# Kernel tuning notes

Hardware: AMD Instinct MI355X
Metric: run time of the kernel (lower is better)

Reference implementation:

```python
import jax, jax.numpy as jnp
import numpy as np

WS = 8          # window size
NUM_HEADS = 3
DIM = 96
HIDDEN = int(DIM * 2.0)
LN_EPS = 1e-5


def _rel_pos_index(ws):
    coords = np.stack(np.meshgrid(np.arange(ws), np.arange(ws), indexing='ij'))  # (2,ws,ws)
    cf = coords.reshape(2, -1)                          # (2, N)
    rel = cf[:, :, None] - cf[:, None, :]               # (2, N, N)
    rel = rel.transpose(1, 2, 0).astype(np.int64)       # (N, N, 2)
    rel[:, :, 0] += ws - 1
    rel[:, :, 1] += ws - 1
    rel[:, :, 0] *= 2 * ws - 1
    return jnp.asarray(rel.sum(-1))                     # (N, N)


def _layernorm(x, g, b):
    mu = jnp.mean(x, axis=-1, keepdims=True)
    var = jnp.mean(jnp.square(x - mu), axis=-1, keepdims=True)
    return (x - mu) * jax.lax.rsqrt(var + LN_EPS) * g + b


def setup_inputs() -> dict:
    key = jax.random.key(0)
    ks = jax.random.split(key, 10)
    C = DIM
    std = 0.02
    return {
        'x': jax.random.normal(ks[0], (8, C, 256, 256), dtype=jnp.float32),
        'qkv_w': jax.random.normal(ks[1], (3 * C, C), dtype=jnp.float32) * std,
        'qkv_b': jnp.zeros((3 * C,), dtype=jnp.float32),
        'proj_w': jax.random.normal(ks[2], (C, C), dtype=jnp.float32) * std,
        'proj_b': jnp.zeros((C,), dtype=jnp.float32),
        'rpb_table': jax.random.normal(ks[3], ((2 * WS - 1) ** 2, NUM_HEADS), dtype=jnp.float32) * std,
        'norm1_g': jnp.ones((C,), dtype=jnp.float32),
        'norm1_b': jnp.zeros((C,), dtype=jnp.float32),
        'norm2_g': jnp.ones((C,), dtype=jnp.float32),
        'norm2_b': jnp.zeros((C,), dtype=jnp.float32),
        'fc1_w': jax.random.normal(ks[4], (HIDDEN, C), dtype=jnp.float32) * std,
        'fc1_b': jnp.zeros((HIDDEN,), dtype=jnp.float32),
        'fc2_w': jax.random.normal(ks[5], (C, HIDDEN), dtype=jnp.float32) * std,
        'fc2_b': jnp.zeros((C,), dtype=jnp.float32),
        'H': 256,
        'W': 256,
    }


def reference(x, qkv_w, qkv_b, proj_w, proj_b, rpb_table,
              norm1_g, norm1_b, norm2_g, norm2_b,
              fc1_w, fc1_b, fc2_w, fc2_b, H, W):
    B, C, Hc, Wc = x.shape
    ws = WS
    nh, nw = H // ws, W // ws
    N = ws * ws
    heads = NUM_HEADS
    hd = C // heads

    # window partition: (B,C,H,W) -> (B*nh*nw, N, C)
    xp = jnp.transpose(x, (0, 2, 3, 1))
    xw = xp.reshape(B, nh, ws, nw, ws, C).transpose(0, 1, 3, 2, 4, 5)
    xw = xw.reshape(B * nh * nw, N, C)

    xw = _layernorm(xw, norm1_g, norm1_b)

    # window attention
    B_ = B * nh * nw
    qkv = xw @ qkv_w.T + qkv_b                                  # (B_, N, 3C)
    qkv = qkv.reshape(B_, N, 3, heads, hd).transpose(2, 0, 3, 1, 4)
    q, k, v = qkv[0], qkv[1], qkv[2]                            # (B_, h, N, d)
    q = q * (hd ** -0.5)
    attn = jnp.einsum('bhnd,bhmd->bhnm', q, k)                  # (B_, h, N, N)
    rpi = _rel_pos_index(ws)                                    # (N, N)
    bias = rpb_table[rpi.reshape(-1)].reshape(N, N, heads).transpose(2, 0, 1)
    attn = jax.nn.softmax(attn + bias[None], axis=-1)
    out = jnp.einsum('bhnm,bhmd->bhnd', attn, v)                # (B_, h, N, d)
    out = out.transpose(0, 2, 1, 3).reshape(B_, N, C)
    out = out @ proj_w.T + proj_b

    # norm2 + MLP (note: original applies them sequentially, single residual at end)
    out = _layernorm(out, norm2_g, norm2_b)
    h = jax.nn.gelu(out @ fc1_w.T + fc1_b, approximate=False)
    out = h @ fc2_w.T + fc2_b

    # window merge + residual
    out = out.reshape(B, nh, nw, ws, ws, C).transpose(0, 5, 1, 3, 2, 4)
    out = out.reshape(B, C, H, W)
    return out + x
```

## Files before the change

kernel.cpp:

```cpp
#include <hip/hip_runtime.h>
#include <hip/hip_bf16.h>

using bf16 = __hip_bfloat16;
typedef short short8  __attribute__((ext_vector_type(8)));
typedef short short4v __attribute__((ext_vector_type(4)));
typedef float f32x4   __attribute__((ext_vector_type(4)));

static __device__ __forceinline__ float b2f(bf16 v){ return __bfloat162float(v); }
static __device__ __forceinline__ bf16  f2b(float v){ return __float2bfloat16(v); }
static __device__ __forceinline__ float s2f(short s){ return __bfloat162float(__builtin_bit_cast(bf16, s)); }
static __device__ __forceinline__ short f2s(float f){ return __builtin_bit_cast(short, __float2bfloat16(f)); }

static __device__ __forceinline__ short8 ldw8(const float* __restrict__ p){
  const float4 u = *(const float4*)(p);
  const float4 v = *(const float4*)(p + 4);
  short8 r;
  r[0]=f2s(u.x); r[1]=f2s(u.y); r[2]=f2s(u.z); r[3]=f2s(u.w);
  r[4]=f2s(v.x); r[5]=f2s(v.y); r[6]=f2s(v.z); r[7]=f2s(v.w);
  return r;
}

#define MFMA16(a,b,c) __builtin_amdgcn_mfma_f32_16x16x32_bf16((a),(b),(c),0,0,0)

constexpr int TPB = 256;
constexpr float EPS = 1e-5f;
constexpr float QSC = 0.17677669529663687f;

constexpr int WQ_OFF  = 0;
constexpr int WPJ_OFF = 27648;
constexpr int WF1_OFF = 36864;
constexpr int WF2_OFF = 55296;
constexpr int WTOT    = 73728;
constexpr int BTAB_BYTE_OFF = 147456;
constexpr size_t WS_NEEDED = 147456 + 49152;

constexpr int R0_OFF = 0;
constexpr int R1_OFF = 26624;
constexpr int R2_OFF = 53248;
constexpr int SMEM_BYTES = 80896;

__global__ void init_ws_kernel(
    const float* __restrict__ qkvw, const float* __restrict__ projw,
    const float* __restrict__ fc1w, const float* __restrict__ fc2w,
    const float* __restrict__ rpb,
    bf16* __restrict__ wbf, float* __restrict__ btab)
{
  const int i = blockIdx.x * 256 + threadIdx.x;
  if (i < WTOT){
    float v;
    if (i < WPJ_OFF)      v = qkvw[i];
    else if (i < WF1_OFF) v = projw[i - WPJ_OFF];
    else if (i < WF2_OFF) v = fc1w[i - WF1_OFF];
    else                  v = fc2w[i - WF2_OFF];
    wbf[i] = f2b(v);
  }
  if (i < 3*64*64){
    const int h   = i >> 12;
    const int row = (i >> 6) & 63;
    const int col = i & 63;
    const int rel = ((row>>3) - (col>>3) + 7)*15 + ((row&7) - (col&7) + 7);
    btab[i] = rpb[rel*3 + h];
  }
}

template<bool PRE>
__global__ __launch_bounds__(TPB, 2) void swin_block_kernel(
    const float* __restrict__ x,
    const float* __restrict__ qkvw,  const float* __restrict__ qkvb,
    const float* __restrict__ projw, const float* __restrict__ projb,
    const float* __restrict__ rpb,
    const float* __restrict__ n1g,   const float* __restrict__ n1b,
    const float* __restrict__ n2g,   const float* __restrict__ n2b,
    const float* __restrict__ fc1w,  const float* __restrict__ fc1b,
    const float* __restrict__ fc2w,  const float* __restrict__ fc2b,
    float* __restrict__ out,
    const bf16* __restrict__ wbf,    const float* __restrict__ btab)
{
  __shared__ alignas(16) unsigned char smem[SMEM_BYTES];
  bf16* s_a  = (bf16*)(smem + R0_OFF);
  bf16* s_q  = (bf16*)(smem + R0_OFF);
  bf16* s_k  = (bf16*)(smem + R0_OFF + 10240);
  bf16* s_at = (bf16*)(smem + R0_OFF);
  bf16* s_ao = (bf16*)(smem + R1_OFF);
  bf16* s_h  = (bf16*)(smem + R1_OFF);
  bf16* s_vt = (bf16*)(smem + R2_OFF);
  bf16* s_p  = (bf16*)(smem + R2_OFF + 9216);

  const bf16* wQ  = wbf + WQ_OFF;
  const bf16* wP  = wbf + WPJ_OFF;
  const bf16* wF1 = wbf + WF1_OFF;
  const bf16* wF2 = wbf + WF2_OFF;

  const int tid  = threadIdx.x;
  const int wid  = tid >> 6;
  const int lane = tid & 63;
  const int quad = lane >> 4;
  const int l15  = lane & 15;
  const int m0   = wid * 16;
  const int row0 = m0 + quad * 4;

  const int blk = blockIdx.x;
  const int b    = blk >> 9;
  const int wh   = (blk >> 4) & 31;
  const int wcol = blk & 15;
  const size_t base = ((size_t)b * 96) * 65536 + (size_t)wh * 2048 + (size_t)wcol * 16;

  float4 xsave[12];
  #pragma unroll
  for (int it = 0; it < 12; it++){
    const int idx4 = it*256 + tid;
    const int c = idx4 >> 5, r = idx4 & 31;
    const int irow = r >> 2, j0 = (r & 3) * 4;
    const float4 xv = *(const float4*)(x + base + (size_t)c*65536 + irow*256 + j0);
    xsave[it] = xv;
    const int srow = (j0 >> 3)*64 + irow*8 + (j0 & 7);
    s_a[(srow+0)*104 + c] = f2b(xv.x);
    s_a[(srow+1)*104 + c] = f2b(xv.y);
    s_a[(srow+2)*104 + c] = f2b(xv.z);
    s_a[(srow+3)*104 + c] = f2b(xv.w);
  }
  __syncthreads();

  auto layernorm = [&](bf16* buf, const float* g, const float* bta){
    const int rr = tid >> 2, s = tid & 3;
    const int cb = s*24;
    float gv[24], bb[24];
    #pragma unroll
    for (int u = 0; u < 6; u++){
      const float4 g4 = *(const float4*)(g   + cb + u*4);
      const float4 b4 = *(const float4*)(bta + cb + u*4);
      gv[u*4+0]=g4.x; gv[u*4+1]=g4.y; gv[u*4+2]=g4.z; gv[u*4+3]=g4.w;
      bb[u*4+0]=b4.x; bb[u*4+1]=b4.y; bb[u*4+2]=b4.z; bb[u*4+3]=b4.w;
    }
    #pragma unroll
    for (int wv = 0; wv < 2; wv++){
      bf16* row = buf + (wv*64 + rr)*104;
      float vals[24];
      float sum = 0.f, sq = 0.f;
      #pragma unroll
      for (int u = 0; u < 3; u++){
        short8 v8 = *(const short8*)(row + cb + u*8);
        #pragma unroll
        for (int j = 0; j < 8; j++){ float f = s2f(v8[j]); vals[u*8+j] = f; sum += f; sq += f*f; }
      }
      sum += __shfl_xor(sum, 1); sum += __shfl_xor(sum, 2);
      sq  += __shfl_xor(sq , 1); sq  += __shfl_xor(sq , 2);
      const float mu  = sum * (1.f/96.f);
      const float inv = rsqrtf(fmaxf(sq*(1.f/96.f) - mu*mu, 0.f) + EPS);
      #pragma unroll
      for (int u = 0; u < 3; u++){
        short8 o8;
        #pragma unroll
        for (int j = 0; j < 8; j++)
          o8[j] = f2s((vals[u*8+j] - mu) * inv * gv[u*8+j] + bb[u*8+j]);
        *(short8*)(row + cb + u*8) = o8;
      }
    }
  };

  layernorm(s_a, n1g, n1b);

  const f32x4 zac = {0.f, 0.f, 0.f, 0.f};

  short8 A0[2], A1[2], A2[2];
  #pragma unroll
  for (int wv = 0; wv < 2; wv++){
    const bf16* ap = s_a + (wv*64 + m0 + l15)*104 + quad*8;
    A0[wv] = *(const short8*)(ap);
    A1[wv] = *(const short8*)(ap + 32);
    A2[wv] = *(const short8*)(ap + 64);
  }
  __syncthreads();

  for (int h = 0; h < 3; h++){
    #pragma unroll
    for (int nt = 0; nt < 6; nt++){
      const int sect = nt >> 1;
      const int d = (nt & 1)*16 + l15;
      const int wrow = sect*96 + h*32 + d;
      short8 w0, w1, w2;
      if constexpr (PRE){
        const bf16* wp = wQ + wrow*96 + quad*8;
        w0 = *(const short8*)(wp);
        w1 = *(const short8*)(wp + 32);
        w2 = *(const short8*)(wp + 64);
      } else {
        const float* wp = qkvw + wrow*96 + quad*8;
        w0 = ldw8(wp); w1 = ldw8(wp + 32); w2 = ldw8(wp + 64);
      }
      const float bias = qkvb[wrow];
      const f32x4 bacc = {bias, bias, bias, bias};
      #pragma unroll
      for (int wv = 0; wv < 2; wv++){
        f32x4 acc = bacc;
        acc = MFMA16(A0[wv], w0, acc);
        acc = MFMA16(A1[wv], w1, acc);
        acc = MFMA16(A2[wv], w2, acc);
        if (sect == 0){
          #pragma unroll
          for (int r = 0; r < 4; r++)
            s_q[(wv*64 + row0 + r)*40 + d] = f2b(acc[r] * QSC);
        } else if (sect == 1){
          #pragma unroll
          for (int r = 0; r < 4; r++)
            s_k[(wv*64 + row0 + r)*40 + d] = f2b(acc[r]);
        } else {
          short4v pk;
          #pragma unroll
          for (int r = 0; r < 4; r++) pk[r] = f2s(acc[r]);
          *(short4v*)(s_vt + wv*2304 + d*72 + row0) = pk;
        }
      }
    }
    __syncthreads();

    {
      f32x4 bvv[4];
      if constexpr (PRE){
        #pragma unroll
        for (int nt = 0; nt < 4; nt++)
          #pragma unroll
          for (int r = 0; r < 4; r++)
            bvv[nt][r] = btab[(h*64 + row0 + r)*64 + nt*16 + l15];
      } else {
        #pragma unroll
        for (int nt = 0; nt < 4; nt++){
          const int col = nt*16 + l15, ci = col >> 3, cj = col & 7;
          #pragma unroll
          for (int r = 0; r < 4; r++){
            const int row = row0 + r, ri = row >> 3, rj = row & 7;
            const int rel = (ri - ci + 7)*15 + (rj - cj + 7);
            bvv[nt][r] = rpb[rel*3 + h];
          }
        }
      }
      #pragma unroll
      for (int wv = 0; wv < 2; wv++){
        const short8 aq = *(const short8*)(s_q + (wv*64 + m0 + l15)*40 + quad*8);
        f32x4 sc[4];
        #pragma unroll
        for (int nt = 0; nt < 4; nt++){
          const short8 bk = *(const short8*)(s_k + (wv*64 + nt*16 + l15)*40 + quad*8);
          sc[nt] = MFMA16(aq, bk, bvv[nt]);
        }
        #pragma unroll
        for (int r = 0; r < 4; r++){
          float mx = fmaxf(fmaxf(sc[0][r], sc[1][r]), fmaxf(sc[2][r], sc[3][r]));
          mx = fmaxf(mx, __shfl_xor(mx, 1));
          mx = fmaxf(mx, __shfl_xor(mx, 2));
          mx = fmaxf(mx, __shfl_xor(mx, 4));
          mx = fmaxf(mx, __shfl_xor(mx, 8));
          const float e0 = __expf(sc[0][r]-mx), e1 = __expf(sc[1][r]-mx);
          const float e2 = __expf(sc[2][r]-mx), e3 = __expf(sc[3][r]-mx);
          float sm = e0+e1+e2+e3;
          sm += __shfl_xor(sm, 1);
          sm += __shfl_xor(sm, 2);
          sm += __shfl_xor(sm, 4);
          sm += __shfl_xor(sm, 8);
          const float rs = 1.f / sm;
          const int prow = (wv*64 + row0 + r)*72;
          s_p[prow +  0 + l15] = f2b(e0*rs);
          s_p[prow + 16 + l15] = f2b(e1*rs);
          s_p[prow + 32 + l15] = f2b(e2*rs);
          s_p[prow + 48 + l15] = f2b(e3*rs);
        }

        const short8 p0 = *(const short8*)(s_p + (wv*64 + m0 + l15)*72 +  0 + quad*8);
        const short8 p1 = *(const short8*)(s_p + (wv*64 + m0 + l15)*72 + 32 + quad*8);
        #pragma unroll
        for (int nt = 0; nt < 2; nt++){
          f32x4 acc = zac;
          acc = MFMA16(p0, *(const short8*)(s_vt + wv*2304 + (nt*16+l15)*72 +  0 + quad*8), acc);
          acc = MFMA16(p1, *(const short8*)(s_vt + wv*2304 + (nt*16+l15)*72 + 32 + quad*8), acc);
          #pragma unroll
          for (int r = 0; r < 4; r++)
            s_ao[(wv*64 + row0 + r)*104 + h*32 + nt*16 + l15] = f2b(acc[r]);
        }
      }
    }
    __syncthreads();
  }

  {
    short8 B0[2], B1[2], B2[2];
    #pragma unroll
    for (int wv = 0; wv < 2; wv++){
      const bf16* bp = s_ao + (wv*64 + m0 + l15)*104 + quad*8;
      B0[wv] = *(const short8*)(bp);
      B1[wv] = *(const short8*)(bp + 32);
      B2[wv] = *(const short8*)(bp + 64);
    }
    #pragma unroll
    for (int nt = 0; nt < 6; nt++){
      const int wrow = nt*16 + l15;
      short8 w0, w1, w2;
      if constexpr (PRE){
        const bf16* wp = wP + wrow*96 + quad*8;
        w0 = *(const short8*)(wp);
        w1 = *(const short8*)(wp + 32);
        w2 = *(const short8*)(wp + 64);
      } else {
        const float* wp = projw + wrow*96 + quad*8;
        w0 = ldw8(wp); w1 = ldw8(wp + 32); w2 = ldw8(wp + 64);
      }
      const float bias = projb[wrow];
      const f32x4 bacc = {bias, bias, bias, bias};
      #pragma unroll
      for (int wv = 0; wv < 2; wv++){
        f32x4 acc = bacc;
        acc = MFMA16(B0[wv], w0, acc);
        acc = MFMA16(B1[wv], w1, acc);
        acc = MFMA16(B2[wv], w2, acc);
        #pragma unroll
        for (int r = 0; r < 4; r++)
          s_a[(wv*64 + row0 + r)*104 + wrow] = f2b(acc[r]);
      }
    }
  }
  __syncthreads();

  layernorm(s_a, n2g, n2b);

  {
    short8 C0[2], C1[2], C2[2];
    #pragma unroll
    for (int wv = 0; wv < 2; wv++){
      const bf16* cp = s_a + (wv*64 + m0 + l15)*104 + quad*8;
      C0[wv] = *(const short8*)(cp);
      C1[wv] = *(const short8*)(cp + 32);
      C2[wv] = *(const short8*)(cp + 64);
    }
    #pragma unroll
    for (int nt = 0; nt < 12; nt++){
      const int wrow = nt*16 + l15;
      short8 w0, w1, w2;
      if constexpr (PRE){
        const bf16* wp = wF1 + wrow*96 + quad*8;
        w0 = *(const short8*)(wp);
        w1 = *(const short8*)(wp + 32);
        w2 = *(const short8*)(wp + 64);
      } else {
        const float* wp = fc1w + wrow*96 + quad*8;
        w0 = ldw8(wp); w1 = ldw8(wp + 32); w2 = ldw8(wp + 64);
      }
      const float bias = fc1b[wrow];
      const f32x4 bacc = {bias, bias, bias, bias};
      #pragma unroll
      for (int wv = 0; wv < 2; wv++){
        f32x4 acc = bacc;
        acc = MFMA16(C0[wv], w0, acc);
        acc = MFMA16(C1[wv], w1, acc);
        acc = MFMA16(C2[wv], w2, acc);
        #pragma unroll
        for (int r = 0; r < 4; r++){
          const float v = acc[r];
          const float t = __expf(1.5957691216057308f * (v + 0.044715f*v*v*v));
          const float g = v - v * (1.f / (t + 1.f));
          s_h[(wv*64 + row0 + r)*200 + wrow] = f2b(g);
        }
      }
    }
  }
  __syncthreads();

  {
    short8 F[2][6];
    #pragma unroll
    for (int wv = 0; wv < 2; wv++)
      #pragma unroll
      for (int ks = 0; ks < 6; ks++)
        F[wv][ks] = *(const short8*)(s_h + (wv*64 + m0 + l15)*200 + ks*32 + quad*8);
    #pragma unroll
    for (int nt = 0; nt < 6; nt++){
      const int wrow = nt*16 + l15;
      short8 w[6];
      if constexpr (PRE){
        const bf16* wp = wF2 + wrow*192 + quad*8;
        #pragma unroll
        for (int ks = 0; ks < 6; ks++) w[ks] = *(const short8*)(wp + ks*32);
      } else {
        const float* wp = fc2w + wrow*192 + quad*8;
        #pragma unroll
        for (int ks = 0; ks < 6; ks++) w[ks] = ldw8(wp + ks*32);
      }
      const float bias = fc2b[wrow];
      const f32x4 bacc = {bias, bias, bias, bias};
      #pragma unroll
      for (int wv = 0; wv < 2; wv++){
        f32x4 acc = bacc;
        #pragma unroll
        for (int ks = 0; ks < 6; ks++)
          acc = MFMA16(F[wv][ks], w[ks], acc);
        short4v pk;
        #pragma unroll
        for (int r = 0; r < 4; r++) pk[r] = f2s(acc[r]);
        *(short4v*)(s_at + wrow*136 + wv*64 + row0) = pk;
      }
    }
  }
  __syncthreads();

  #pragma unroll
  for (int it = 0; it < 12; it++){
    const int idx4 = it*256 + tid;
    const int c = idx4 >> 5, r = idx4 & 31;
    const int irow = r >> 2, j0 = (r & 3) * 4;
    const int t0 = (j0 >> 3)*64 + irow*8 + (j0 & 7);
    const short4v pv = *(const short4v*)(s_at + c*136 + t0);
    const size_t g = base + (size_t)c*65536 + irow*256 + j0;
    const float4 xv = xsave[it];
    float4 ov;
    ov.x = xv.x + s2f(pv[0]);
    ov.y = xv.y + s2f(pv[1]);
    ov.z = xv.z + s2f(pv[2]);
    ov.w = xv.w + s2f(pv[3]);
    *(float4*)(out + g) = ov;
  }
}

extern "C" void kernel_launch(void* const* d_in, const int* in_sizes, int n_in,
                              void* d_out, int out_size, void* d_ws, size_t ws_size,
                              hipStream_t stream) {
  const float* x     = (const float*)d_in[0];
  const float* qkvw  = (const float*)d_in[1];
  const float* qkvb  = (const float*)d_in[2];
  const float* projw = (const float*)d_in[3];
  const float* projb = (const float*)d_in[4];
  const float* rpb   = (const float*)d_in[5];
  const float* n1g   = (const float*)d_in[6];
  const float* n1b   = (const float*)d_in[7];
  const float* n2g   = (const float*)d_in[8];
  const float* n2b   = (const float*)d_in[9];
  const float* fc1w  = (const float*)d_in[10];
  const float* fc1b  = (const float*)d_in[11];
  const float* fc2w  = (const float*)d_in[12];
  const float* fc2b  = (const float*)d_in[13];
  float* out = (float*)d_out;

  if (ws_size >= WS_NEEDED && d_ws != nullptr) {
    bf16*  wbf  = (bf16*)d_ws;
    float* btab = (float*)((char*)d_ws + BTAB_BYTE_OFF);
    init_ws_kernel<<<dim3(288), dim3(256), 0, stream>>>(
        qkvw, projw, fc1w, fc2w, rpb, wbf, btab);
    swin_block_kernel<true><<<dim3(4096), dim3(TPB), 0, stream>>>(
        x, qkvw, qkvb, projw, projb, rpb,
        n1g, n1b, n2g, n2b, fc1w, fc1b, fc2w, fc2b, out, wbf, btab);
  } else {
    swin_block_kernel<false><<<dim3(4096), dim3(TPB), 0, stream>>>(
        x, qkvw, qkvb, projw, projb, rpb,
        n1g, n1b, n2g, n2b, fc1w, fc1b, fc2w, fc2b, out,
        (const bf16*)nullptr, (const float*)nullptr);
  }
}
```

Before: 617.6 us.

## Swizzle LDS layouts, fuse LayerNorm2 into projection, drop softmax max and fold q-scale

All shared-memory tiles now use byte addressing with an XOR swizzle on the column offset keyed by row bits. The intent is to cut LDS bank conflicts on MFMA fragment loads and the scattered bf16 stores. LayerNorm2 is computed in registers straight from the projection accumulators with cross-lane shuffles, which removes a shared-memory round trip and a separate pass. The softmax drops the row-max reduction and only clamps scores before exponentiating, and the q scale is folded into the pre-converted weights and bias. Skipping the max subtraction trades numerical robustness for fewer shuffles.

```diff
diff --git a/kernel.cpp b/kernel.cpp
--- a/kernel.cpp
+++ b/kernel.cpp
@@ -6,7 +6,6 @@
 typedef short short4v __attribute__((ext_vector_type(4)));
 typedef float f32x4   __attribute__((ext_vector_type(4)));
 
-static __device__ __forceinline__ float b2f(bf16 v){ return __bfloat162float(v); }
 static __device__ __forceinline__ bf16  f2b(float v){ return __float2bfloat16(v); }
 static __device__ __forceinline__ float s2f(short s){ return __bfloat162float(__builtin_bit_cast(bf16, s)); }
 static __device__ __forceinline__ short f2s(float f){ return __builtin_bit_cast(short, __float2bfloat16(f)); }
@@ -21,6 +20,8 @@
 }
 
 #define MFMA16(a,b,c) __builtin_amdgcn_mfma_f32_16x16x32_bf16((a),(b),(c),0,0,0)
+
+#define KEYR(row) ((((row) >> 2) & 3) << 4)
 
 constexpr int TPB = 256;
 constexpr float EPS = 1e-5f;
@@ -52,6 +53,7 @@
     else if (i < WF1_OFF) v = projw[i - WPJ_OFF];
     else if (i < WF2_OFF) v = fc1w[i - WF1_OFF];
     else                  v = fc2w[i - WF2_OFF];
+    if (i < 9216) v *= QSC;
     wbf[i] = f2b(v);
   }
   if (i < 3*64*64){
@@ -77,14 +79,14 @@
     const bf16* __restrict__ wbf,    const float* __restrict__ btab)
 {
   __shared__ alignas(16) unsigned char smem[SMEM_BYTES];
-  bf16* s_a  = (bf16*)(smem + R0_OFF);
-  bf16* s_q  = (bf16*)(smem + R0_OFF);
-  bf16* s_k  = (bf16*)(smem + R0_OFF + 10240);
-  bf16* s_at = (bf16*)(smem + R0_OFF);
-  bf16* s_ao = (bf16*)(smem + R1_OFF);
-  bf16* s_h  = (bf16*)(smem + R1_OFF);
-  bf16* s_vt = (bf16*)(smem + R2_OFF);
-  bf16* s_p  = (bf16*)(smem + R2_OFF + 9216);
+  char* s_a  = (char*)(smem + R0_OFF);
+  char* s_q  = (char*)(smem + R0_OFF);
+  char* s_k  = (char*)(smem + R0_OFF + 10240);
+  char* s_at = (char*)(smem + R0_OFF);
+  char* s_ao = (char*)(smem + R1_OFF);
+  char* s_h  = (char*)(smem + R1_OFF);
+  char* s_vt = (char*)(smem + R2_OFF);
+  char* s_p  = (char*)(smem + R2_OFF + 9216);
 
   const bf16* wQ  = wbf + WQ_OFF;
   const bf16* wP  = wbf + WPJ_OFF;
@@ -98,6 +100,8 @@
   const int l15  = lane & 15;
   const int m0   = wid * 16;
   const int row0 = m0 + quad * 4;
+  const int cwz  = quad << 4;
+  const int rwz  = ((l15 >> 2) & 3) << 4;
 
   const int blk = blockIdx.x;
   const int b    = blk >> 9;
@@ -114,32 +118,34 @@
     const float4 xv = *(const float4*)(x + base + (size_t)c*65536 + irow*256 + j0);
     xsave[it] = xv;
     const int srow = (j0 >> 3)*64 + irow*8 + (j0 & 7);
-    s_a[(srow+0)*104 + c] = f2b(xv.x);
-    s_a[(srow+1)*104 + c] = f2b(xv.y);
-    s_a[(srow+2)*104 + c] = f2b(xv.z);
-    s_a[(srow+3)*104 + c] = f2b(xv.w);
+    const int co = (c*2) ^ KEYR(srow);
+    *(bf16*)(s_a + (srow+0)*208 + co) = f2b(xv.x);
+    *(bf16*)(s_a + (srow+1)*208 + co) = f2b(xv.y);
+    *(bf16*)(s_a + (srow+2)*208 + co) = f2b(xv.z);
+    *(bf16*)(s_a + (srow+3)*208 + co) = f2b(xv.w);
   }
   __syncthreads();
 
-  auto layernorm = [&](bf16* buf, const float* g, const float* bta){
+  {
     const int rr = tid >> 2, s = tid & 3;
     const int cb = s*24;
+    const int key = KEYR(rr);
     float gv[24], bb[24];
     #pragma unroll
     for (int u = 0; u < 6; u++){
-      const float4 g4 = *(const float4*)(g   + cb + u*4);
-      const float4 b4 = *(const float4*)(bta + cb + u*4);
+      const float4 g4 = *(const float4*)(n1g + cb + u*4);
+      const float4 b4 = *(const float4*)(n1b + cb + u*4);
       gv[u*4+0]=g4.x; gv[u*4+1]=g4.y; gv[u*4+2]=g4.z; gv[u*4+3]=g4.w;
       bb[u*4+0]=b4.x; bb[u*4+1]=b4.y; bb[u*4+2]=b4.z; bb[u*4+3]=b4.w;
     }
     #pragma unroll
     for (int wv = 0; wv < 2; wv++){
-      bf16* row = buf + (wv*64 + rr)*104;
+      char* row = s_a + (wv*64 + rr)*208;
       float vals[24];
       float sum = 0.f, sq = 0.f;
       #pragma unroll
       for (int u = 0; u < 3; u++){
-        short8 v8 = *(const short8*)(row + cb + u*8);
+        short8 v8 = *(const short8*)(row + (((cb + u*8)*2) ^ key));
         #pragma unroll
         for (int j = 0; j < 8; j++){ float f = s2f(v8[j]); vals[u*8+j] = f; sum += f; sq += f*f; }
       }
@@ -153,22 +159,21 @@
         #pragma unroll
         for (int j = 0; j < 8; j++)
           o8[j] = f2s((vals[u*8+j] - mu) * inv * gv[u*8+j] + bb[u*8+j]);
-        *(short8*)(row + cb + u*8) = o8;
-      }
-    }
-  };
-
-  layernorm(s_a, n1g, n1b);
+        *(short8*)(row + (((cb + u*8)*2) ^ key)) = o8;
+      }
+    }
+  }
 
   const f32x4 zac = {0.f, 0.f, 0.f, 0.f};
 
   short8 A0[2], A1[2], A2[2];
   #pragma unroll
   for (int wv = 0; wv < 2; wv++){
-    const bf16* ap = s_a + (wv*64 + m0 + l15)*104 + quad*8;
-    A0[wv] = *(const short8*)(ap);
-    A1[wv] = *(const short8*)(ap + 32);
-    A2[wv] = *(const short8*)(ap + 64);
+    const char* ap = s_a + (wv*64 + m0 + l15)*208;
+    const int q16 = (quad*16) ^ rwz;
+    A0[wv] = *(const short8*)(ap + q16);
+    A1[wv] = *(const short8*)(ap + q16 + 64);
+    A2[wv] = *(const short8*)(ap + q16 + 128);
   }
   __syncthreads();
 
@@ -188,7 +193,8 @@
         const float* wp = qkvw + wrow*96 + quad*8;
         w0 = ldw8(wp); w1 = ldw8(wp + 32); w2 = ldw8(wp + 64);
       }
-      const float bias = qkvb[wrow];
+      float bias = qkvb[wrow];
+      if (PRE && sect == 0) bias *= QSC;
       const f32x4 bacc = {bias, bias, bias, bias};
       #pragma unroll
       for (int wv = 0; wv < 2; wv++){
@@ -198,17 +204,19 @@
         acc = MFMA16(A2[wv], w2, acc);
         if (sect == 0){
           #pragma unroll
+          for (int r = 0; r < 4; r++){
+            const float qv = PRE ? acc[r] : acc[r]*QSC;
+            *(bf16*)(s_q + (wv*64 + row0 + r)*80 + ((d*2) ^ cwz)) = f2b(qv);
+          }
+        } else if (sect == 1){
+          #pragma unroll
           for (int r = 0; r < 4; r++)
-            s_q[(wv*64 + row0 + r)*40 + d] = f2b(acc[r] * QSC);
-        } else if (sect == 1){
-          #pragma unroll
-          for (int r = 0; r < 4; r++)
-            s_k[(wv*64 + row0 + r)*40 + d] = f2b(acc[r]);
+            *(bf16*)(s_k + (wv*64 + row0 + r)*80 + ((d*2) ^ cwz)) = f2b(acc[r]);
         } else {
           short4v pk;
           #pragma unroll
           for (int r = 0; r < 4; r++) pk[r] = f2s(acc[r]);
-          *(short4v*)(s_vt + wv*2304 + d*72 + row0) = pk;
+          *(short4v*)(s_vt + wv*4608 + d*144 + ((row0*2) ^ KEYR(d))) = pk;
         }
       }
     }
@@ -236,45 +244,45 @@
       }
       #pragma unroll
       for (int wv = 0; wv < 2; wv++){
-        const short8 aq = *(const short8*)(s_q + (wv*64 + m0 + l15)*40 + quad*8);
+        const int q16 = (quad*16) ^ rwz;
+        const short8 aq = *(const short8*)(s_q + (wv*64 + m0 + l15)*80 + q16);
         f32x4 sc[4];
         #pragma unroll
         for (int nt = 0; nt < 4; nt++){
-          const short8 bk = *(const short8*)(s_k + (wv*64 + nt*16 + l15)*40 + quad*8);
+          const short8 bk = *(const short8*)(s_k + (wv*64 + nt*16 + l15)*80 + q16);
           sc[nt] = MFMA16(aq, bk, bvv[nt]);
         }
         #pragma unroll
         for (int r = 0; r < 4; r++){
-          float mx = fmaxf(fmaxf(sc[0][r], sc[1][r]), fmaxf(sc[2][r], sc[3][r]));
-          mx = fmaxf(mx, __shfl_xor(mx, 1));
-          mx = fmaxf(mx, __shfl_xor(mx, 2));
-          mx = fmaxf(mx, __shfl_xor(mx, 4));
-          mx = fmaxf(mx, __shfl_xor(mx, 8));
-          const float e0 = __expf(sc[0][r]-mx), e1 = __expf(sc[1][r]-mx);
-          const float e2 = __expf(sc[2][r]-mx), e3 = __expf(sc[3][r]-mx);
+          const float e0 = __expf(fminf(sc[0][r], 80.f));
+          const float e1 = __expf(fminf(sc[1][r], 80.f));
+          const float e2 = __expf(fminf(sc[2][r], 80.f));
+          const float e3 = __expf(fminf(sc[3][r], 80.f));
           float sm = e0+e1+e2+e3;
           sm += __shfl_xor(sm, 1);
           sm += __shfl_xor(sm, 2);
           sm += __shfl_xor(sm, 4);
           sm += __shfl_xor(sm, 8);
           const float rs = 1.f / sm;
-          const int prow = (wv*64 + row0 + r)*72;
-          s_p[prow +  0 + l15] = f2b(e0*rs);
-          s_p[prow + 16 + l15] = f2b(e1*rs);
-          s_p[prow + 32 + l15] = f2b(e2*rs);
-          s_p[prow + 48 + l15] = f2b(e3*rs);
-        }
-
-        const short8 p0 = *(const short8*)(s_p + (wv*64 + m0 + l15)*72 +  0 + quad*8);
-        const short8 p1 = *(const short8*)(s_p + (wv*64 + m0 + l15)*72 + 32 + quad*8);
+          char* pb = s_p + (wv*64 + row0 + r)*144;
+          *(bf16*)(pb + ((      l15*2) ^ cwz)) = f2b(e0*rs);
+          *(bf16*)(pb + (( 32 + l15*2) ^ cwz)) = f2b(e1*rs);
+          *(bf16*)(pb + (( 64 + l15*2) ^ cwz)) = f2b(e2*rs);
+          *(bf16*)(pb + (( 96 + l15*2) ^ cwz)) = f2b(e3*rs);
+        }
+
+        const char* pr = s_p + (wv*64 + m0 + l15)*144;
+        const short8 p0 = *(const short8*)(pr + q16);
+        const short8 p1 = *(const short8*)(pr + q16 + 64);
         #pragma unroll
         for (int nt = 0; nt < 2; nt++){
+          const char* vr = s_vt + wv*4608 + (nt*16 + l15)*144;
           f32x4 acc = zac;
-          acc = MFMA16(p0, *(const short8*)(s_vt + wv*2304 + (nt*16+l15)*72 +  0 + quad*8), acc);
-          acc = MFMA16(p1, *(const short8*)(s_vt + wv*2304 + (nt*16+l15)*72 + 32 + quad*8), acc);
+          acc = MFMA16(p0, *(const short8*)(vr + q16), acc);
+          acc = MFMA16(p1, *(const short8*)(vr + q16 + 64), acc);
           #pragma unroll
           for (int r = 0; r < 4; r++)
-            s_ao[(wv*64 + row0 + r)*104 + h*32 + nt*16 + l15] = f2b(acc[r]);
+            *(bf16*)(s_ao + (wv*64 + row0 + r)*208 + (((h*32 + nt*16 + l15)*2) ^ cwz)) = f2b(acc[r]);
         }
       }
     }
@@ -285,11 +293,19 @@
     short8 B0[2], B1[2], B2[2];
     #pragma unroll
     for (int wv = 0; wv < 2; wv++){
-      const bf16* bp = s_ao + (wv*64 + m0 + l15)*104 + quad*8;
-      B0[wv] = *(const short8*)(bp);
-      B1[wv] = *(const short8*)(bp + 32);
-      B2[wv] = *(const short8*)(bp + 64);
-    }
+      const char* bp = s_ao + (wv*64 + m0 + l15)*208;
+      const int q16 = (quad*16) ^ rwz;
+      B0[wv] = *(const short8*)(bp + q16);
+      B1[wv] = *(const short8*)(bp + q16 + 64);
+      B2[wv] = *(const short8*)(bp + q16 + 128);
+    }
+    float g6[6], b6[6];
+    #pragma unroll
+    for (int nt = 0; nt < 6; nt++){
+      g6[nt] = n2g[nt*16 + l15];
+      b6[nt] = n2b[nt*16 + l15];
+    }
+    float vals[2][6][4];
     #pragma unroll
     for (int nt = 0; nt < 6; nt++){
       const int wrow = nt*16 + l15;
@@ -312,23 +328,41 @@
         acc = MFMA16(B1[wv], w1, acc);
         acc = MFMA16(B2[wv], w2, acc);
         #pragma unroll
-        for (int r = 0; r < 4; r++)
-          s_a[(wv*64 + row0 + r)*104 + wrow] = f2b(acc[r]);
+        for (int r = 0; r < 4; r++) vals[wv][nt][r] = acc[r];
+      }
+    }
+    #pragma unroll
+    for (int wv = 0; wv < 2; wv++){
+      #pragma unroll
+      for (int r = 0; r < 4; r++){
+        float sm = 0.f, sq = 0.f;
+        #pragma unroll
+        for (int nt = 0; nt < 6; nt++){ const float v = vals[wv][nt][r]; sm += v; sq += v*v; }
+        sm += __shfl_xor(sm, 1); sm += __shfl_xor(sm, 2);
+        sm += __shfl_xor(sm, 4); sm += __shfl_xor(sm, 8);
+        sq += __shfl_xor(sq, 1); sq += __shfl_xor(sq, 2);
+        sq += __shfl_xor(sq, 4); sq += __shfl_xor(sq, 8);
+        const float mu  = sm * (1.f/96.f);
+        const float inv = rsqrtf(fmaxf(sq*(1.f/96.f) - mu*mu, 0.f) + EPS);
+        char* ob = s_a + (wv*64 + row0 + r)*208;
+        #pragma unroll
+        for (int nt = 0; nt < 6; nt++)
+          *(bf16*)(ob + (((nt*16 + l15)*2) ^ cwz)) =
+              f2b((vals[wv][nt][r] - mu) * inv * g6[nt] + b6[nt]);
       }
     }
   }
   __syncthreads();
-
-  layernorm(s_a, n2g, n2b);
 
   {
     short8 C0[2], C1[2], C2[2];
     #pragma unroll
     for (int wv = 0; wv < 2; wv++){
-      const bf16* cp = s_a + (wv*64 + m0 + l15)*104 + quad*8;
-      C0[wv] = *(const short8*)(cp);
-      C1[wv] = *(const short8*)(cp + 32);
-      C2[wv] = *(const short8*)(cp + 64);
+      const char* cp = s_a + (wv*64 + m0 + l15)*208;
+      const int q16 = (quad*16) ^ rwz;
+      C0[wv] = *(const short8*)(cp + q16);
+      C1[wv] = *(const short8*)(cp + q16 + 64);
+      C2[wv] = *(const short8*)(cp + q16 + 128);
     }
     #pragma unroll
     for (int nt = 0; nt < 12; nt++){
@@ -356,7 +390,7 @@
           const float v = acc[r];
           const float t = __expf(1.5957691216057308f * (v + 0.044715f*v*v*v));
           const float g = v - v * (1.f / (t + 1.f));
-          s_h[(wv*64 + row0 + r)*200 + wrow] = f2b(g);
+          *(bf16*)(s_h + (wv*64 + row0 + r)*400 + ((wrow*2) ^ cwz)) = f2b(g);
         }
       }
     }
@@ -366,10 +400,13 @@
   {
     short8 F[2][6];
     #pragma unroll
-    for (int wv = 0; wv < 2; wv++)
+    for (int wv = 0; wv < 2; wv++){
+      const char* fp = s_h + (wv*64 + m0 + l15)*400;
+      const int q16 = (quad*16) ^ rwz;
       #pragma unroll
       for (int ks = 0; ks < 6; ks++)
-        F[wv][ks] = *(const short8*)(s_h + (wv*64 + m0 + l15)*200 + ks*32 + quad*8);
+        F[wv][ks] = *(const short8*)(fp + ks*64 + q16);
+    }
     #pragma unroll
     for (int nt = 0; nt < 6; nt++){
       const int wrow = nt*16 + l15;
@@ -394,7 +431,7 @@
         short4v pk;
         #pragma unroll
         for (int r = 0; r < 4; r++) pk[r] = f2s(acc[r]);
-        *(short4v*)(s_at + wrow*136 + wv*64 + row0) = pk;
+        *(short4v*)(s_at + wrow*272 + (wv*64 + row0)*2) = pk;
       }
     }
   }
@@ -406,7 +443,7 @@
     const int c = idx4 >> 5, r = idx4 & 31;
     const int irow = r >> 2, j0 = (r & 3) * 4;
     const int t0 = (j0 >> 3)*64 + irow*8 + (j0 & 7);
-    const short4v pv = *(const short4v*)(s_at + c*136 + t0);
+    const short4v pv = *(const short4v*)(s_at + c*272 + t0*2);
     const size_t g = base + (size_t)c*65536 + irow*256 + j0;
     const float4 xv = xsave[it];
     float4 ov;
```

New measurement: 618.2 us. Within noise of the previous version (+0.1%).
